# Performance work log

Hardware: AMD Instinct MI355X
Metric: run time of the kernel (lower is better)

Reference implementation:

```python
import jax, jax.numpy as jnp
import numpy as np

IN_NC = 512

def setup_inputs() -> dict:
    key = jax.random.key(0)
    k1, k2, k3, k4 = jax.random.split(key, 4)
    B, N = 8, 2048
    nd, out_nc = 512, 512
    x = jax.random.normal(k1, (B, N * IN_NC), dtype=jnp.float32)
    # store weights as [in_nc, d] so projection is x @ W (same math as torch Linear with W^T)
    Wq = jax.random.normal(k2, (IN_NC, nd), dtype=jnp.float32) * (1.0 / np.sqrt(IN_NC))
    Wk = jax.random.normal(k3, (IN_NC, nd), dtype=jnp.float32) * (1.0 / np.sqrt(IN_NC))
    Wv = jax.random.normal(k4, (IN_NC, out_nc), dtype=jnp.float32) * (1.0 / np.sqrt(IN_NC))
    return {"x": x, "Wq": Wq, "Wk": Wk, "Wv": Wv}

def reference(x, Wq, Wk, Wv):
    B = x.shape[0]
    N = x.shape[1] // IN_NC
    xt = x.reshape(B, N, IN_NC)                     # [B, N, in_nc]
    Q = jnp.einsum('bnc,cd->bnd', xt, Wq)           # [B, N, nd]
    K = jnp.einsum('bnc,cd->bnd', xt, Wk)           # [B, N, nd]
    V = jnp.einsum('bnc,cd->bnd', xt, Wv)           # [B, N, out_nc]
    A = jnp.einsum('bnd,bmd->bnm', Q, K)            # [B, N, N]  (no scale, as in source)
    A = jax.nn.softmax(A, axis=-1)
    out = jnp.einsum('bnm,bmd->bnd', A, V)          # [B, N, out_nc]
    return out.reshape(B, -1)
```

## Files before the change

### kernel.cpp

```cpp
#include <hip/hip_runtime.h>
#include <hip/hip_fp16.h>

typedef _Float16 f16x8 __attribute__((ext_vector_type(8)));
typedef _Float16 f16x4 __attribute__((ext_vector_type(4)));
typedef float    f32x4 __attribute__((ext_vector_type(4)));

#define LOG2E 1.44269504f

__device__ __forceinline__ void stage128x64(const _Float16* __restrict__ g, int ld,
                                            void* lds, int tid)
{
    const int r0   = tid >> 3;
    const int colh = ((tid & 7) ^ (r0 & 7)) << 3;
    char* lbase = (char*)lds + (tid >> 6) * 1024;
#pragma unroll
    for (int i = 0; i < 4; i++) {
        const _Float16* src = g + (size_t)(i * 32 + r0) * ld + colh;
        __builtin_amdgcn_global_load_lds(
            (const __attribute__((address_space(1))) void*)src,
            (__attribute__((address_space(3))) void*)(lbase + i * 4096),
            16, 0, 0);
    }
}

__device__ __forceinline__ f16x8 lds_frag(const void* lds, int row, int colh)
{
    const int off = row * 128 + ((colh * 2) ^ ((row & 7) << 4));
    return *(const f16x8*)((const char*)lds + off);
}

template<int NK>
__device__ __forceinline__ void gemm_loop_cv(const _Float16* __restrict__ A, int lda,
                                             const _Float16* __restrict__ B, int ldb,
                                             _Float16* a0, _Float16* a1,
                                             _Float16* b0, _Float16* b1,
                                             f32x4 acc[4][4], int tid,
                                             int wr, int wc, int lrow, int lkg)
{
    stage128x64(A, lda, a0, tid);
    stage128x64(B, ldb, b0, tid);
    stage128x64(A + 64, lda, a1, tid);
    stage128x64(B + 64, ldb, b1, tid);
    asm volatile("s_waitcnt vmcnt(8)" ::: "memory");
    __builtin_amdgcn_s_barrier();
    __builtin_amdgcn_sched_barrier(0);

    for (int t = 0; t < NK; ++t) {
        _Float16* acur = (t & 1) ? a1 : a0;
        _Float16* bcur = (t & 1) ? b1 : b0;

        f16x8 af[2][4], bf[2][4];
#pragma unroll
        for (int kk = 0; kk < 2; kk++) {
#pragma unroll
            for (int mi = 0; mi < 4; mi++)
                af[kk][mi] = lds_frag(acur, wr * 64 + mi * 16 + lrow, kk * 32 + lkg * 8);
#pragma unroll
            for (int ni = 0; ni < 4; ni++)
                bf[kk][ni] = lds_frag(bcur, wc * 64 + ni * 16 + lrow, kk * 32 + lkg * 8);
        }
        asm volatile("s_waitcnt lgkmcnt(0)" ::: "memory");
        __builtin_amdgcn_sched_barrier(0);
        __builtin_amdgcn_s_barrier();

        if (t + 2 < NK) {
            stage128x64(A + (size_t)(t + 2) * 64, lda, acur, tid);
            stage128x64(B + (size_t)(t + 2) * 64, ldb, bcur, tid);
        }
        __builtin_amdgcn_sched_barrier(0);

        __builtin_amdgcn_s_setprio(1);
#pragma unroll
        for (int kk = 0; kk < 2; kk++)
#pragma unroll
            for (int mi = 0; mi < 4; mi++)
#pragma unroll
                for (int ni = 0; ni < 4; ni++)
                    acc[mi][ni] = __builtin_amdgcn_mfma_f32_16x16x32_f16(
                        af[kk][mi], bf[kk][ni], acc[mi][ni], 0, 0, 0);
        __builtin_amdgcn_s_setprio(0);

        if (t + 2 < NK) asm volatile("s_waitcnt vmcnt(8)" ::: "memory");
        else            asm volatile("s_waitcnt vmcnt(0)" ::: "memory");
        __builtin_amdgcn_sched_barrier(0);
        __builtin_amdgcn_s_barrier();
        __builtin_amdgcn_sched_barrier(0);
    }
}

__global__ __launch_bounds__(256)
void convert_kernel(const float* __restrict__ x,
                    const float* __restrict__ Wq,
                    const float* __restrict__ Wk,
                    const float* __restrict__ Wv,
                    _Float16* __restrict__ xh,
                    _Float16* __restrict__ Wt)
{
    const int b = blockIdx.x;
    if (b < 2048) {
        const size_t base = (size_t)b * 4096 + (size_t)threadIdx.x * 4;
#pragma unroll
        for (int i = 0; i < 4; i++) {
            f32x4 v = *(const f32x4*)(x + base + i * 1024);
            f16x4 h;
#pragma unroll
            for (int j = 0; j < 4; j++) h[j] = (_Float16)v[j];
            *(f16x4*)(xh + base + i * 1024) = h;
        }
    } else {
        __shared__ float tb[32][33];
        const int t = b - 2048;
        const int mat = t >> 8;
        const int tile = t & 255;
        const int tr = tile >> 4, tc = tile & 15;
        const float* W = (mat == 0) ? Wq : (mat == 1) ? Wk : Wv;
        const int r = threadIdx.x >> 5, c = threadIdx.x & 31;
#pragma unroll
        for (int p = 0; p < 4; p++)
            tb[p * 8 + r][c] = W[(size_t)(tr * 32 + p * 8 + r) * 512 + tc * 32 + c];
        __syncthreads();
#pragma unroll
        for (int p = 0; p < 4; p++)
            Wt[((size_t)mat * 512 + tc * 32 + p * 8 + r) * 512 + tr * 32 + c] =
                (_Float16)tb[c][p * 8 + r];
    }
}

__global__ __launch_bounds__(256, 2)
void proj_kernel(const _Float16* __restrict__ xh,
                 const _Float16* __restrict__ Wt,
                 _Float16* __restrict__ Qf,
                 _Float16* __restrict__ Kf,
                 _Float16* __restrict__ Vt)
{
    __shared__ _Float16 a0[128 * 64], a1[128 * 64];
    __shared__ _Float16 b0[128 * 64], b1[128 * 64];

    const int tid = threadIdx.x;
    const int mb = blockIdx.x, cb = blockIdx.y;
    const int mat = cb >> 2, nb = cb & 3;
    const int m0 = mb * 128, n0 = nb * 128;

    const _Float16* Abase = xh + (size_t)m0 * 512;
    const _Float16* Bbase = Wt + ((size_t)mat * 512 + n0) * 512;

    const int lane = tid & 63;
    const int w = tid >> 6;
    const int wr = w >> 1, wc = w & 1;
    const int lrow = lane & 15, lkg = lane >> 4;

    f32x4 acc[4][4];
#pragma unroll
    for (int i = 0; i < 4; i++)
#pragma unroll
        for (int j = 0; j < 4; j++) acc[i][j] = (f32x4)0.0f;

    gemm_loop_cv<8>(Abase, 512, Bbase, 512, a0, a1, b0, b1,
                    acc, tid, wr, wc, lrow, lkg);

    if (mat < 2) {
        _Float16* Out = (mat == 0) ? Qf : Kf;
#pragma unroll
        for (int mi = 0; mi < 4; mi++) {
            const int mbase = m0 + wr * 64 + mi * 16 + lkg * 4;
#pragma unroll
            for (int ni = 0; ni < 4; ni++) {
                const int ncol = n0 + wc * 64 + ni * 16 + lrow;
#pragma unroll
                for (int r = 0; r < 4; r++)
                    Out[(size_t)(mbase + r) * 512 + ncol] = (_Float16)acc[mi][ni][r];
            }
        }
    } else {
#pragma unroll
        for (int mi = 0; mi < 4; mi++) {
            const int mglob = m0 + wr * 64 + mi * 16 + lkg * 4;
            const int b = mglob >> 11, mloc = mglob & 2047;
#pragma unroll
            for (int ni = 0; ni < 4; ni++) {
                const int d = n0 + wc * 64 + ni * 16 + lrow;
                f16x4 h;
#pragma unroll
                for (int r = 0; r < 4; r++) h[r] = (_Float16)acc[mi][ni][r];
                *(f16x4*)&Vt[((size_t)b * 512 + d) * 2048 + mloc] = h;
            }
        }
    }
}

__global__ __launch_bounds__(256, 2)
void score_kernel(const _Float16* __restrict__ Qf,
                  const _Float16* __restrict__ Kf,
                  _Float16* __restrict__ P,
                  float2* __restrict__ ML, int b0)
{
    __shared__ __align__(16) char smem[65536];
    _Float16* a0  = (_Float16*)smem;
    _Float16* a1  = (_Float16*)(smem + 16384);
    _Float16* b0p = (_Float16*)(smem + 32768);
    _Float16* b1p = (_Float16*)(smem + 49152);
    float (*S_lds)[132] = (float(*)[132])smem;

    const int tid = threadIdx.x;
    const int bl = blockIdx.x, mb = blockIdx.y, nb = blockIdx.z;
    const int bg = b0 + bl;

    const _Float16* Abase = Qf + (size_t)(bg * 2048 + nb * 128) * 512;
    const _Float16* Bbase = Kf + (size_t)(bg * 2048 + mb * 128) * 512;

    const int lane = tid & 63;
    const int w = tid >> 6;
    const int wr = w >> 1, wc = w & 1;
    const int lrow = lane & 15, lkg = lane >> 4;

    f32x4 acc[4][4];
#pragma unroll
    for (int i = 0; i < 4; i++)
#pragma unroll
        for (int j = 0; j < 4; j++) acc[i][j] = (f32x4)0.0f;

    gemm_loop_cv<8>(Abase, 512, Bbase, 512, a0, a1, b0p, b1p,
                    acc, tid, wr, wc, lrow, lkg);

    _Float16* Pb = P + (size_t)bl * 2048 * 2048;
    const int s  = tid >> 2;
    const int q4 = tid & 3;

#pragma unroll
    for (int hp = 0; hp < 2; hp++) {
#pragma unroll
        for (int m2 = 0; m2 < 2; m2++) {
            const int mi = hp * 2 + m2;
            const int srow = wr * 32 + m2 * 16 + lkg * 4;
#pragma unroll
            for (int ni = 0; ni < 4; ni++) {
                const int col = wc * 64 + ni * 16 + lrow;
#pragma unroll
                for (int rr = 0; rr < 4; rr++)
                    S_lds[srow + rr][col] = acc[mi][ni][rr];
            }
        }
        __syncthreads();

        f32x4 vv[8];
#pragma unroll
        for (int seg = 0; seg < 4; seg++) {
            vv[seg * 2 + 0] = *(const f32x4*)&S_lds[s][q4 * 8 + seg * 32 + 0];
            vv[seg * 2 + 1] = *(const f32x4*)&S_lds[s][q4 * 8 + seg * 32 + 4];
        }

        float m = vv[0][0];
#pragma unroll
        for (int j = 0; j < 8; j++)
#pragma unroll
            for (int jj = 0; jj < 4; jj++) m = fmaxf(m, vv[j][jj]);
        m = fmaxf(m, __shfl_xor(m, 1));
        m = fmaxf(m, __shfl_xor(m, 2));

        float l = 0.0f;
#pragma unroll
        for (int j = 0; j < 8; j++)
#pragma unroll
            for (int jj = 0; jj < 4; jj++) {
                float e = exp2f((vv[j][jj] - m) * LOG2E);
                vv[j][jj] = e;
                l += e;
            }
        l += __shfl_xor(l, 1);
        l += __shfl_xor(l, 2);

        const int q_local = (s >> 5) * 64 + hp * 32 + (s & 31);
        const int q = nb * 128 + q_local;

        if (q4 == 0) {
            float2 v; v.x = m; v.y = l;
            ML[((size_t)bl * 2048 + q) * 16 + mb] = v;
        }

#pragma unroll
        for (int seg = 0; seg < 4; seg++) {
            f16x8 h;
#pragma unroll
            for (int jj = 0; jj < 4; jj++) {
                h[jj]     = (_Float16)vv[seg * 2 + 0][jj];
                h[jj + 4] = (_Float16)vv[seg * 2 + 1][jj];
            }
            *(f16x8*)&Pb[(size_t)q * 2048 + mb * 128 + q4 * 8 + seg * 32] = h;
        }
        if (hp == 0) __syncthreads();
    }
}

__global__ __launch_bounds__(256, 2)
void out_kernel(const _Float16* __restrict__ P,
                const _Float16* __restrict__ Vt,
                const float2* __restrict__ ML,
                float* __restrict__ out, int b0)
{
    __shared__ _Float16 a0[128 * 64], a1[128 * 64];
    __shared__ _Float16 b0p[128 * 64], b1p[128 * 64];
    __shared__ float scale_lds[128][17];

    const int tid = threadIdx.x;
    const int bl = blockIdx.x;
    const int db = blockIdx.y >> 4, nb = blockIdx.y & 15;
    const int bg = b0 + bl;

    if (tid < 128) {
        const float2* mlrow = ML + ((size_t)bl * 2048 + nb * 128 + tid) * 16;
        float2 ml[16];
        float M = -3.4e38f;
#pragma unroll
        for (int t = 0; t < 16; t++) { ml[t] = mlrow[t]; M = fmaxf(M, ml[t].x); }
        float L = 0.0f;
#pragma unroll
        for (int t = 0; t < 16; t++) L += ml[t].y * exp2f((ml[t].x - M) * LOG2E);
        const float invL = 1.0f / L;
#pragma unroll
        for (int t = 0; t < 16; t++)
            scale_lds[tid][t] = exp2f((ml[t].x - M) * LOG2E) * invL;
    }

    const _Float16* Abase = P  + (size_t)bl * 2048 * 2048 + (size_t)(nb * 128) * 2048;
    const _Float16* Bbase = Vt + (size_t)bg * 512  * 2048 + (size_t)(db * 128) * 2048;

    const int lane = tid & 63;
    const int w = tid >> 6;
    const int wr = w >> 1, wc = w & 1;
    const int lrow = lane & 15, lkg = lane >> 4;

    f32x4 acc[4][4];
#pragma unroll
    for (int i = 0; i < 4; i++)
#pragma unroll
        for (int j = 0; j < 4; j++) acc[i][j] = (f32x4)0.0f;

    __syncthreads();

    stage128x64(Abase,      2048, a0,  tid);
    stage128x64(Bbase,      2048, b0p, tid);
    stage128x64(Abase + 64, 2048, a1,  tid);
    stage128x64(Bbase + 64, 2048, b1p, tid);
    asm volatile("s_waitcnt vmcnt(8)" ::: "memory");
    __builtin_amdgcn_s_barrier();
    __builtin_amdgcn_sched_barrier(0);

    for (int t = 0; t < 32; ++t) {
        _Float16* acur = (t & 1) ? a1 : a0;
        _Float16* bcur = (t & 1) ? b1p : b0p;
        const int kt = t >> 1;

        f16x8 af[2][4], bf[2][4];
        float sc[4];
#pragma unroll
        for (int kk = 0; kk < 2; kk++) {
#pragma unroll
            for (int mi = 0; mi < 4; mi++)
                af[kk][mi] = lds_frag(acur, wr * 64 + mi * 16 + lrow, kk * 32 + lkg * 8);
#pragma unroll
            for (int ni = 0; ni < 4; ni++)
                bf[kk][ni] = lds_frag(bcur, wc * 64 + ni * 16 + lrow, kk * 32 + lkg * 8);
        }
#pragma unroll
        for (int mi = 0; mi < 4; mi++)
            sc[mi] = scale_lds[wr * 64 + mi * 16 + lrow][kt];
        asm volatile("s_waitcnt lgkmcnt(0)" ::: "memory");
        __builtin_amdgcn_sched_barrier(0);
        __builtin_amdgcn_s_barrier();

        if (t + 2 < 32) {
            stage128x64(Abase + (size_t)(t + 2) * 64, 2048, acur, tid);
            stage128x64(Bbase + (size_t)(t + 2) * 64, 2048, bcur, tid);
        }
        __builtin_amdgcn_sched_barrier(0);

        __builtin_amdgcn_s_setprio(1);
#pragma unroll
        for (int kk = 0; kk < 2; kk++)
#pragma unroll
            for (int mi = 0; mi < 4; mi++) {
                const f16x8 a = af[kk][mi] * (_Float16)sc[mi];
#pragma unroll
                for (int ni = 0; ni < 4; ni++)
                    acc[mi][ni] = __builtin_amdgcn_mfma_f32_16x16x32_f16(
                        a, bf[kk][ni], acc[mi][ni], 0, 0, 0);
            }
        __builtin_amdgcn_s_setprio(0);

        if (t + 2 < 32) asm volatile("s_waitcnt vmcnt(8)" ::: "memory");
        else            asm volatile("s_waitcnt vmcnt(0)" ::: "memory");
        __builtin_amdgcn_sched_barrier(0);
        __builtin_amdgcn_s_barrier();
        __builtin_amdgcn_sched_barrier(0);
    }

#pragma unroll
    for (int mi = 0; mi < 4; mi++) {
        const int nbase = nb * 128 + wr * 64 + mi * 16 + lkg * 4;
#pragma unroll
        for (int ni = 0; ni < 4; ni++) {
            const int d = db * 128 + wc * 64 + ni * 16 + lrow;
#pragma unroll
            for (int rr = 0; rr < 4; rr++)
                out[((size_t)bg * 2048 + nbase + rr) * 512 + d] = acc[mi][ni][rr];
        }
    }
}

extern "C" void kernel_launch(void* const* d_in, const int* in_sizes, int n_in,
                              void* d_out, int out_size, void* d_ws, size_t ws_size,
                              hipStream_t stream) {
    const float* x  = (const float*)d_in[0];
    const float* Wq = (const float*)d_in[1];
    const float* Wk = (const float*)d_in[2];
    const float* Wv = (const float*)d_in[3];

    const size_t MB = 1024ull * 1024ull;
    char* ws = (char*)d_ws;
    _Float16* Qf = (_Float16*)ws;
    _Float16* Kf = Qf + (size_t)16384 * 512;
    _Float16* Vt = Kf + (size_t)16384 * 512;
    _Float16* P  = Vt + (size_t)16384 * 512;
    float*    out = (float*)d_out;

    int chunk;
    if      (ws_size >= 120 * MB) chunk = 8;
    else if (ws_size >= 88  * MB) chunk = 4;
    else if (ws_size >= 70  * MB) chunk = 2;
    else                          chunk = 1;

    float2* ML = (float2*)(P + (size_t)chunk * 2048 * 2048);

    _Float16* xh = (_Float16*)P;
    _Float16* Wt = xh + (size_t)16384 * 512;

    convert_kernel<<<2816, 256, 0, stream>>>(x, Wq, Wk, Wv, xh, Wt);
    proj_kernel<<<dim3(128, 12), 256, 0, stream>>>(xh, Wt, Qf, Kf, Vt);

    for (int b0 = 0; b0 < 8; b0 += chunk) {
        score_kernel<<<dim3(chunk, 16, 16), 256, 0, stream>>>(Qf, Kf, P, ML, b0);
        out_kernel<<<dim3(chunk, 64), 256, 0, stream>>>(P, Vt, ML, out, b0);
    }
}
```

Baseline: 132.4 us.

## Process two key tiles per score block and prefetch next K during softmax

Each score_kernel block now computes two consecutive 128-key tiles instead of one, and the grid's key dimension is halved to match. The GEMM loop is inlined with explicit async LDS staging and waitcnt control. The next tile's K fragments are prefetched into the B buffers while the first tile's softmax epilogue runs, which hides load latency behind the epilogue. The padded score scratch buffer is replaced by an unpadded XOR-swizzled layout, keeping LDS bank conflicts low without the padding. The costs are fewer blocks in flight, serialized per-block work, and fragile hand-tuned vmcnt counts.

```diff
diff --git a/kernel.cpp b/kernel.cpp
--- a/kernel.cpp
+++ b/kernel.cpp
@@ -188,6 +188,8 @@
     }
 }
 
+#define SSWZ(r) (((r) & 7) << 2)
+
 __global__ __launch_bounds__(256, 2)
 void score_kernel(const _Float16* __restrict__ Qf,
                   const _Float16* __restrict__ Kf,
@@ -199,95 +201,159 @@
     _Float16* a1  = (_Float16*)(smem + 16384);
     _Float16* b0p = (_Float16*)(smem + 32768);
     _Float16* b1p = (_Float16*)(smem + 49152);
-    float (*S_lds)[132] = (float(*)[132])smem;
+    float (*S_lds)[128] = (float(*)[128])smem;
 
     const int tid = threadIdx.x;
-    const int bl = blockIdx.x, mb = blockIdx.y, nb = blockIdx.z;
+    const int bl = blockIdx.x, mbp = blockIdx.y, nb = blockIdx.z;
     const int bg = b0 + bl;
 
     const _Float16* Abase = Qf + (size_t)(bg * 2048 + nb * 128) * 512;
-    const _Float16* Bbase = Kf + (size_t)(bg * 2048 + mb * 128) * 512;
 
     const int lane = tid & 63;
     const int w = tid >> 6;
     const int wr = w >> 1, wc = w & 1;
     const int lrow = lane & 15, lkg = lane >> 4;
 
-    f32x4 acc[4][4];
-#pragma unroll
-    for (int i = 0; i < 4; i++)
-#pragma unroll
-        for (int j = 0; j < 4; j++) acc[i][j] = (f32x4)0.0f;
-
-    gemm_loop_cv<8>(Abase, 512, Bbase, 512, a0, a1, b0p, b1p,
-                    acc, tid, wr, wc, lrow, lkg);
-
     _Float16* Pb = P + (size_t)bl * 2048 * 2048;
     const int s  = tid >> 2;
     const int q4 = tid & 3;
 
-#pragma unroll
-    for (int hp = 0; hp < 2; hp++) {
-#pragma unroll
-        for (int m2 = 0; m2 < 2; m2++) {
-            const int mi = hp * 2 + m2;
-            const int srow = wr * 32 + m2 * 16 + lkg * 4;
-#pragma unroll
-            for (int ni = 0; ni < 4; ni++) {
-                const int col = wc * 64 + ni * 16 + lrow;
-#pragma unroll
-                for (int rr = 0; rr < 4; rr++)
-                    S_lds[srow + rr][col] = acc[mi][ni][rr];
-            }
-        }
-        __syncthreads();
-
-        f32x4 vv[8];
-#pragma unroll
-        for (int seg = 0; seg < 4; seg++) {
-            vv[seg * 2 + 0] = *(const f32x4*)&S_lds[s][q4 * 8 + seg * 32 + 0];
-            vv[seg * 2 + 1] = *(const f32x4*)&S_lds[s][q4 * 8 + seg * 32 + 4];
-        }
-
-        float m = vv[0][0];
-#pragma unroll
-        for (int j = 0; j < 8; j++)
-#pragma unroll
-            for (int jj = 0; jj < 4; jj++) m = fmaxf(m, vv[j][jj]);
-        m = fmaxf(m, __shfl_xor(m, 1));
-        m = fmaxf(m, __shfl_xor(m, 2));
-
-        float l = 0.0f;
-#pragma unroll
-        for (int j = 0; j < 8; j++)
-#pragma unroll
-            for (int jj = 0; jj < 4; jj++) {
-                float e = exp2f((vv[j][jj] - m) * LOG2E);
-                vv[j][jj] = e;
-                l += e;
-            }
-        l += __shfl_xor(l, 1);
-        l += __shfl_xor(l, 2);
-
-        const int q_local = (s >> 5) * 64 + hp * 32 + (s & 31);
-        const int q = nb * 128 + q_local;
-
-        if (q4 == 0) {
-            float2 v; v.x = m; v.y = l;
-            ML[((size_t)bl * 2048 + q) * 16 + mb] = v;
-        }
-
-#pragma unroll
-        for (int seg = 0; seg < 4; seg++) {
-            f16x8 h;
-#pragma unroll
-            for (int jj = 0; jj < 4; jj++) {
-                h[jj]     = (_Float16)vv[seg * 2 + 0][jj];
-                h[jj + 4] = (_Float16)vv[seg * 2 + 1][jj];
-            }
-            *(f16x8*)&Pb[(size_t)q * 2048 + mb * 128 + q4 * 8 + seg * 32] = h;
-        }
-        if (hp == 0) __syncthreads();
+    for (int half = 0; half < 2; ++half) {
+        const int mb = mbp * 2 + half;
+        const _Float16* Bbase = Kf + (size_t)(bg * 2048 + mb * 128) * 512;
+
+        if (half == 0) {
+            stage128x64(Abase,      512, a0,  tid);
+            stage128x64(Bbase,      512, b0p, tid);
+            stage128x64(Abase + 64, 512, a1,  tid);
+            stage128x64(Bbase + 64, 512, b1p, tid);
+            asm volatile("s_waitcnt vmcnt(8)" ::: "memory");
+        } else {
+            stage128x64(Abase,      512, a0, tid);
+            stage128x64(Abase + 64, 512, a1, tid);
+            asm volatile("s_waitcnt vmcnt(4)" ::: "memory");
+        }
+        __builtin_amdgcn_s_barrier();
+        __builtin_amdgcn_sched_barrier(0);
+
+        f32x4 acc[4][4];
+#pragma unroll
+        for (int i = 0; i < 4; i++)
+#pragma unroll
+            for (int j = 0; j < 4; j++) acc[i][j] = (f32x4)0.0f;
+
+        for (int t = 0; t < 8; ++t) {
+            _Float16* acur = (t & 1) ? a1 : a0;
+            _Float16* bcur = (t & 1) ? b1p : b0p;
+
+            f16x8 af[2][4], bf[2][4];
+#pragma unroll
+            for (int kk = 0; kk < 2; kk++) {
+#pragma unroll
+                for (int mi = 0; mi < 4; mi++)
+                    af[kk][mi] = lds_frag(acur, wr * 64 + mi * 16 + lrow, kk * 32 + lkg * 8);
+#pragma unroll
+                for (int ni = 0; ni < 4; ni++)
+                    bf[kk][ni] = lds_frag(bcur, wc * 64 + ni * 16 + lrow, kk * 32 + lkg * 8);
+            }
+            asm volatile("s_waitcnt lgkmcnt(0)" ::: "memory");
+            __builtin_amdgcn_sched_barrier(0);
+            __builtin_amdgcn_s_barrier();
+
+            if (t + 2 < 8) {
+                stage128x64(Abase + (size_t)(t + 2) * 64, 512, acur, tid);
+                stage128x64(Bbase + (size_t)(t + 2) * 64, 512, bcur, tid);
+            }
+            __builtin_amdgcn_sched_barrier(0);
+
+            __builtin_amdgcn_s_setprio(1);
+#pragma unroll
+            for (int kk = 0; kk < 2; kk++)
+#pragma unroll
+                for (int mi = 0; mi < 4; mi++)
+#pragma unroll
+                    for (int ni = 0; ni < 4; ni++)
+                        acc[mi][ni] = __builtin_amdgcn_mfma_f32_16x16x32_f16(
+                            af[kk][mi], bf[kk][ni], acc[mi][ni], 0, 0, 0);
+            __builtin_amdgcn_s_setprio(0);
+
+            if (t + 2 < 8) asm volatile("s_waitcnt vmcnt(8)" ::: "memory");
+            else           asm volatile("s_waitcnt vmcnt(0)" ::: "memory");
+            __builtin_amdgcn_sched_barrier(0);
+            __builtin_amdgcn_s_barrier();
+            __builtin_amdgcn_sched_barrier(0);
+        }
+
+        if (half == 0) {
+            const _Float16* Bn = Kf + (size_t)(bg * 2048 + (mb + 1) * 128) * 512;
+            stage128x64(Bn,      512, b0p, tid);
+            stage128x64(Bn + 64, 512, b1p, tid);
+        }
+        __builtin_amdgcn_sched_barrier(0);
+
+#pragma unroll
+        for (int hp = 0; hp < 2; hp++) {
+#pragma unroll
+            for (int m2 = 0; m2 < 2; m2++) {
+                const int mi = hp * 2 + m2;
+                const int srow = wr * 32 + m2 * 16 + lkg * 4;
+#pragma unroll
+                for (int ni = 0; ni < 4; ni++) {
+                    const int col = wc * 64 + ni * 16 + lrow;
+#pragma unroll
+                    for (int rr = 0; rr < 4; rr++)
+                        S_lds[srow + rr][col ^ SSWZ(srow + rr)] = acc[mi][ni][rr];
+                }
+            }
+            __syncthreads();
+
+            f32x4 vv[8];
+#pragma unroll
+            for (int seg = 0; seg < 4; seg++) {
+                vv[seg * 2 + 0] = *(const f32x4*)&S_lds[s][(q4 * 8 + seg * 32 + 0) ^ SSWZ(s)];
+                vv[seg * 2 + 1] = *(const f32x4*)&S_lds[s][(q4 * 8 + seg * 32 + 4) ^ SSWZ(s)];
+            }
+
+            float m = vv[0][0];
+#pragma unroll
+            for (int j = 0; j < 8; j++)
+#pragma unroll
+                for (int jj = 0; jj < 4; jj++) m = fmaxf(m, vv[j][jj]);
+            m = fmaxf(m, __shfl_xor(m, 1));
+            m = fmaxf(m, __shfl_xor(m, 2));
+
+            float l = 0.0f;
+#pragma unroll
+            for (int j = 0; j < 8; j++)
+#pragma unroll
+                for (int jj = 0; jj < 4; jj++) {
+                    float e = exp2f((vv[j][jj] - m) * LOG2E);
+                    vv[j][jj] = e;
+                    l += e;
+                }
+            l += __shfl_xor(l, 1);
+            l += __shfl_xor(l, 2);
+
+            const int q_local = (s >> 5) * 64 + hp * 32 + (s & 31);
+            const int q = nb * 128 + q_local;
+
+            if (q4 == 0) {
+                float2 v; v.x = m; v.y = l;
+                ML[((size_t)bl * 2048 + q) * 16 + mb] = v;
+            }
+
+#pragma unroll
+            for (int seg = 0; seg < 4; seg++) {
+                f16x8 h;
+#pragma unroll
+                for (int jj = 0; jj < 4; jj++) {
+                    h[jj]     = (_Float16)vv[seg * 2 + 0][jj];
+                    h[jj + 4] = (_Float16)vv[seg * 2 + 1][jj];
+                }
+                *(f16x8*)&Pb[(size_t)q * 2048 + mb * 128 + q4 * 8 + seg * 32] = h;
+            }
+            if (hp == 0 || half == 0) __syncthreads();
+        }
     }
 }
 
@@ -438,7 +504,7 @@
     proj_kernel<<<dim3(128, 12), 256, 0, stream>>>(xh, Wt, Qf, Kf, Vt);
 
     for (int b0 = 0; b0 < 8; b0 += chunk) {
-        score_kernel<<<dim3(chunk, 16, 16), 256, 0, stream>>>(Qf, Kf, P, ML, b0);
+        score_kernel<<<dim3(chunk, 8, 16), 256, 0, stream>>>(Qf, Kf, P, ML, b0);
         out_kernel<<<dim3(chunk, 64), 256, 0, stream>>>(P, Vt, ML, out, b0);
     }
 }
```

Result: slower. 147.6 us (+11.5%).
